# Performance work log

Measured on AMD Instinct MI355X. Metric: run time of the kernel, lower is better.

The kernel has to match this reference:

```python
import jax, jax.numpy as jnp
import numpy as np
from jax import lax

# Dimensions (must match input_specs)
B, T, C = 2, 2048, 1024
H = 4 * C          # FFN hidden
E_RWKV, E_TRANS = 6, 2
E = E_RWKV + E_TRANS
LN_EPS = 1e-5


def layernorm(x, g, b):
    m = x.mean(-1, keepdims=True)
    v = ((x - m) ** 2).mean(-1, keepdims=True)
    return (x - m) * lax.rsqrt(v + LN_EPS) * g + b


def setup_inputs() -> dict:
    key = jax.random.key(0)
    ks = jax.random.split(key, 24)
    s = 0.02
    inp = {
        "x": jax.random.normal(ks[0], (B, T, C), jnp.float32),
        "v_first": jax.random.normal(ks[1], (B, T, C), jnp.float32),
        "winners": jax.random.randint(ks[2], (B, T, 2), 0, E),
        "capital_shares": jax.random.uniform(ks[3], (E,), jnp.float32),
        # LayerNorms
        "ln1_g": jnp.ones((C,), jnp.float32), "ln1_b": jnp.zeros((C,), jnp.float32),
        "ln2_g": jnp.ones((C,), jnp.float32), "ln2_b": jnp.zeros((C,), jnp.float32),
        # RWKV-style time-mix (simplified RWKV7_TimeMix)
        "Wr": s * jax.random.normal(ks[4], (C, C), jnp.float32),
        "Wk": s * jax.random.normal(ks[5], (C, C), jnp.float32),
        "Wv": s * jax.random.normal(ks[6], (C, C), jnp.float32),
        "Wo": s * jax.random.normal(ks[7], (C, C), jnp.float32),
        "w_decay": jax.random.normal(ks[8], (C,), jnp.float32),
        "g_v": jax.random.normal(ks[9], (C,), jnp.float32),
        # bridge: linear on concat(h, rwkv_state)
        "Wb": s * jax.random.normal(ks[10], (2 * C, C), jnp.float32),
        "bb": jnp.zeros((C,), jnp.float32),
        # 6 stacked SparseRWKVFFN experts: sigmoid(x Wr_r) * (relu(x Wk_r)^2 Wv_r)
        "Wk_r": s * jax.random.normal(ks[11], (E_RWKV, C, H), jnp.float32),
        "Wv_r": s * jax.random.normal(ks[12], (E_RWKV, H, C), jnp.float32),
        "Wr_r": s * jax.random.normal(ks[13], (E_RWKV, C, C), jnp.float32),
        # 2 stacked LinearTransformerExpert: gelu((h+prefix) W1) W2
        "W1_t": s * jax.random.normal(ks[14], (E_TRANS, C, H), jnp.float32),
        "W2_t": s * jax.random.normal(ks[15], (E_TRANS, H, C), jnp.float32),
    }
    return inp


def reference(x, v_first, winners, capital_shares,
              ln1_g, ln1_b, ln2_g, ln2_b,
              Wr, Wk, Wv, Wo, w_decay, g_v,
              Wb, bb, Wk_r, Wv_r, Wr_r, W1_t, W2_t):
    # ---- attention (simplified RWKV time-mix), returns per-token state ----
    h1 = layernorm(x, ln1_g, ln1_b)
    r = jax.nn.sigmoid(h1 @ Wr)                      # [B,T,C]
    k = h1 @ Wk
    v = h1 @ Wv
    v = v + (v_first - v) * jax.nn.sigmoid(g_v)      # value-residual mix
    w = jax.nn.sigmoid(w_decay)                      # per-channel decay [C]

    def step(s, kv):
        k_t, v_t = kv                                # [B,C] each
        s = w * s + k_t * v_t
        return s, s

    s0 = jnp.zeros((B, C), x.dtype)
    _, states = lax.scan(step, s0, (jnp.swapaxes(k, 0, 1), jnp.swapaxes(v, 0, 1)))
    states = jnp.swapaxes(states, 0, 1)              # rwkv_state [B,T,C]

    att_out = (r * states) @ Wo
    x = x + att_out
    h = layernorm(x, ln2_g, ln2_b)

    # ---- bridge prefix (flat over tokens, vectorized) ----
    bridge_prefix = jnp.concatenate([h, states], axis=-1) @ Wb + bb  # [B,T,C]

    # ---- experts computed densely, combined by top-2 gates ----
    # RWKV FFN experts
    a = jnp.square(jax.nn.relu(jnp.einsum('btc,ech->ebth', h, Wk_r)))     # [Er,B,T,H]
    rec = jax.nn.sigmoid(jnp.einsum('btc,ecd->ebtd', h, Wr_r))            # [Er,B,T,C]
    out_r = rec * jnp.einsum('ebth,ehc->ebtc', a, Wv_r)                   # [Er,B,T,C]
    # Linear-transformer experts consume the bridge prefix
    ht = h + bridge_prefix
    out_t = jnp.einsum('ebth,ehc->ebtc',
                       jax.nn.gelu(jnp.einsum('btc,ech->ebth', ht, W1_t)),
                       W2_t)                                              # [Et,B,T,C]
    all_out = jnp.concatenate([out_r, out_t], axis=0)                     # [E,B,T,C]

    # top-2 combine, each rank weighted 0.5 (use_market=False branch)
    gate = 0.5 * (jax.nn.one_hot(winners[..., 0], E, dtype=x.dtype)
                  + jax.nn.one_hot(winners[..., 1], E, dtype=x.dtype))    # [B,T,E]
    final_out = jnp.einsum('ebtc,bte->btc', all_out, gate)

    return x + final_out
```

## Files before the change

### kernel.cpp

```cpp
#include <hip/hip_runtime.h>

typedef unsigned short u16;
typedef __bf16 bf16x8 __attribute__((ext_vector_type(8)));
typedef float f32x4 __attribute__((ext_vector_type(4)));

__device__ __forceinline__ float bf2f(u16 u){ union{unsigned i;float f;}x; x.i=((unsigned)u)<<16; return x.f; }
__device__ __forceinline__ u16 f2bf(float f){ union{float f;unsigned i;}x; x.f=f; unsigned r = x.i + 0x7FFFu + ((x.i>>16)&1u); return (u16)(r>>16); }
__device__ __forceinline__ float sigm(float x){ return 1.f/(1.f+expf(-x)); }

struct __align__(8) U16x4 { u16 v[4]; };

#define PSTRIDE 8388608ull

struct CJob { const float* src; u16* dst; int K, N, base; };
struct CJobs { CJob j[27]; };

__global__ void conv_all(CJobs cj){
  __shared__ u16 tile[128][65];
  int id = blockIdx.x;
  int sel = 0;
  #pragma unroll
  for (int i=1;i<27;++i) if (cj.j[i].base <= id) sel = i;
  const float* __restrict__ src = cj.j[sel].src;
  u16* __restrict__ dst = cj.j[sel].dst;
  int K = cj.j[sel].K, N = cj.j[sel].N;
  int lt = id - cj.j[sel].base;
  int tn = N >> 6;
  int k0 = (lt / tn) * 128, n0 = (lt % tn) * 64;
  int tid = threadIdx.x;
  #pragma unroll
  for (int it=0; it<8; ++it){
    int e = it*1024 + tid*4;
    int r = e>>6, c = e&63;
    float4 v = *(const float4*)(src + (size_t)(k0+r)*N + n0 + c);
    tile[r][c+0]=f2bf(v.x); tile[r][c+1]=f2bf(v.y); tile[r][c+2]=f2bf(v.z); tile[r][c+3]=f2bf(v.w);
  }
  __syncthreads();
  #pragma unroll
  for (int it=0; it<8; ++it){
    int e = it*1024 + tid*4;
    int n = e>>7, k = e&127;
    U16x4 o;
    #pragma unroll
    for (int j=0;j<4;++j) o.v[j] = tile[k+j][n];
    *(U16x4*)(dst + (size_t)(n0+n)*K + k0 + k) = o;
  }
}

__global__ void ln_k(const float* __restrict__ x, const float* __restrict__ g, const float* __restrict__ b,
                     u16* __restrict__ out, int ostride){
  int row = blockIdx.x, tid = threadIdx.x;
  float4 v = *(const float4*)(x + (size_t)row*1024 + tid*4);
  float s = v.x+v.y+v.z+v.w;
  float ss = v.x*v.x+v.y*v.y+v.z*v.z+v.w*v.w;
  #pragma unroll
  for (int o=32;o;o>>=1){ s += __shfl_down(s,o); ss += __shfl_down(ss,o); }
  __shared__ float sm[8];
  int lane = tid&63, wv = tid>>6;
  if (!lane){ sm[wv]=s; sm[4+wv]=ss; }
  __syncthreads();
  s = sm[0]+sm[1]+sm[2]+sm[3]; ss = sm[4]+sm[5]+sm[6]+sm[7];
  float mean = s*(1.f/1024.f);
  float var = ss*(1.f/1024.f) - mean*mean;
  float inv = rsqrtf(var + 1e-5f);
  U16x4 o;
  const float* vp = &v.x;
  #pragma unroll
  for (int j=0;j<4;++j){
    int c = tid*4+j;
    o.v[j] = f2bf((vp[j]-mean)*inv*g[c] + b[c]);
  }
  *(U16x4*)(out + (size_t)row*ostride + tid*4) = o;
}

__global__ void red_x_ln(const float* __restrict__ x, const u16* __restrict__ part,
                         const float* __restrict__ g, const float* __restrict__ b,
                         float* __restrict__ out, u16* __restrict__ hcat){
  int row = blockIdx.x, tid = threadIdx.x;
  size_t i = (size_t)row*1024 + tid*4;
  U16x4 p0 = *(const U16x4*)(part + i);
  U16x4 p1 = *(const U16x4*)(part + PSTRIDE + i);
  float4 xv = *(const float4*)(x + i);
  float4 v;
  v.x = xv.x + bf2f(p0.v[0]) + bf2f(p1.v[0]);
  v.y = xv.y + bf2f(p0.v[1]) + bf2f(p1.v[1]);
  v.z = xv.z + bf2f(p0.v[2]) + bf2f(p1.v[2]);
  v.w = xv.w + bf2f(p0.v[3]) + bf2f(p1.v[3]);
  *(float4*)(out + i) = v;
  float s = v.x+v.y+v.z+v.w;
  float ss = v.x*v.x+v.y*v.y+v.z*v.z+v.w*v.w;
  #pragma unroll
  for (int o=32;o;o>>=1){ s += __shfl_down(s,o); ss += __shfl_down(ss,o); }
  __shared__ float sm[8];
  int lane = tid&63, wv = tid>>6;
  if (!lane){ sm[wv]=s; sm[4+wv]=ss; }
  __syncthreads();
  s = sm[0]+sm[1]+sm[2]+sm[3]; ss = sm[4]+sm[5]+sm[6]+sm[7];
  float mean = s*(1.f/1024.f);
  float var = ss*(1.f/1024.f) - mean*mean;
  float inv = rsqrtf(var + 1e-5f);
  U16x4 o;
  const float* vp = &v.x;
  #pragma unroll
  for (int j=0;j<4;++j){
    int c = tid*4+j;
    o.v[j] = f2bf((vp[j]-mean)*inv*g[c] + b[c]);
  }
  *(U16x4*)(hcat + (size_t)row*2048 + tid*4) = o;
}

__global__ void scan_p1(const u16* __restrict__ kbuf, const u16* __restrict__ vbuf,
                        const float* __restrict__ w_decay, float* __restrict__ carry){
  int c = blockIdx.x*256 + threadIdx.x;
  int chunk = blockIdx.y, b = blockIdx.z;
  float w = sigm(w_decay[c]);
  float s = 0.f;
  size_t idx = ((size_t)(b*2048 + chunk*64))*1024 + c;
  #pragma unroll 4
  for (int i=0;i<64;++i){ s = w*s + bf2f(kbuf[idx])*bf2f(vbuf[idx]); idx += 1024; }
  carry[((size_t)(b*32+chunk))*1024 + c] = s;
}
__global__ void scan_p2(const float* __restrict__ w_decay, const float* __restrict__ carry,
                        float* __restrict__ startv){
  int c = blockIdx.x*256 + threadIdx.x;
  int b = blockIdx.y;
  float w = sigm(w_decay[c]);
  float wL = w;
  #pragma unroll
  for (int i=0;i<6;++i) wL *= wL;
  float p = 0.f;
  for (int j=0;j<32;++j){
    size_t id = ((size_t)(b*32+j))*1024 + c;
    startv[id] = p;
    p = wL*p + carry[id];
  }
}
__global__ void scan_p3(const u16* __restrict__ kbuf, const u16* __restrict__ vbuf, const u16* __restrict__ rbuf,
                        const float* __restrict__ w_decay, const float* __restrict__ startv,
                        u16* __restrict__ rs, u16* __restrict__ hcat){
  int c = blockIdx.x*256 + threadIdx.x;
  int chunk = blockIdx.y, b = blockIdx.z;
  float w = sigm(w_decay[c]);
  float s = startv[((size_t)(b*32+chunk))*1024 + c];
  size_t t0 = (size_t)b*2048 + chunk*64;
  size_t idx = t0*1024 + c;
  size_t idx2 = t0*2048 + 1024 + c;
  for (int i=0;i<64;++i){
    s = w*s + bf2f(kbuf[idx])*bf2f(vbuf[idx]);
    rs[idx] = f2bf(bf2f(rbuf[idx]) * s);
    hcat[idx2] = f2bf(s);
    idx += 1024; idx2 += 2048;
  }
}

__global__ void route_count(const int* __restrict__ winners, int* __restrict__ offs, int* __restrict__ cursor){
  __shared__ int cnt[8];
  if (threadIdx.x < 8) cnt[threadIdx.x] = 0;
  __syncthreads();
  for (int p = threadIdx.x; p < 8192; p += 256) atomicAdd(&cnt[winners[p]&7], 1);
  __syncthreads();
  if (threadIdx.x == 0){
    int s = 0;
    #pragma unroll
    for (int e=0;e<8;++e){ offs[e]=s; s+=cnt[e]; }
    offs[8]=s;
  }
  if (threadIdx.x < 8) cursor[threadIdx.x] = 0;
}
__global__ void route_scatter(const int* __restrict__ winners, const int* __restrict__ offs,
                              int* __restrict__ cursor, int* __restrict__ idx_all){
  int p = blockIdx.x*256 + threadIdx.x;
  if (p < 8192){
    int e = winners[p]&7;
    int pos = offs[e] + atomicAdd(&cursor[e], 1);
    idx_all[pos] = p>>1;
  }
}

struct GArgs {
  const u16* A; const u16* B;
  long long lda, bstride;
  int K, Mdense, eBase, nxt, kdiv;
  const int* offs; const int* idx_all;
  const float* v_first; const float* g_v;
  u16* rbuf; u16* kbuf; u16* vbuf;
  u16* act; u16* part;
};

#define GLL(gp, lp) __builtin_amdgcn_global_load_lds((const __attribute__((address_space(1))) void*)(gp), \
                                                     (__attribute__((address_space(3))) void*)(lp), 16, 0, 0)

template<int EPI, int GATHER>
__global__ __launch_bounds__(256,3) void gemm_k(GArgs g){
  int e = g.eBase + blockIdx.z;
  int rbase = 0, m = g.Mdense;
  if (g.offs){ rbase = g.offs[e]; m = g.offs[e+1] - rbase; }
  if ((int)blockIdx.y * 128 >= m) return;
  const int xt = (int)blockIdx.x % g.nxt;
  const int ksplit = (int)blockIdx.x / g.nxt;
  const long long kOff = (long long)ksplit * g.kdiv;
  __shared__ char smem[49152];
  const int tid = threadIdx.x, lane = tid&63, wave = tid>>6;
  const int wr = wave>>1, wc = wave&1;
  const int nk = g.kdiv >> 5;

  const int srowi = tid>>2;
  const long long scol = (long long)((tid&3)*8);

  const u16* bBase0 = g.B + (long long)blockIdx.z*g.bstride
                    + ((long long)(xt*128) + srowi)*(long long)g.K + kOff + scol;
  const u16* bBase1 = bBase0 + 64ll*(long long)g.K;

  int aRd[4], bRd[4];
  #pragma unroll
  for (int q=0;q<4;++q){
    aRd[q] = (wr*64 + q*16 + (lane&15))*64 + (lane>>4)*16;
    bRd[q] = 8192 + (wc*64 + q*16 + (lane&15))*64 + (lane>>4)*16;
  }

  for (int mt = blockIdx.y; mt*128 < m; mt += gridDim.y){
    const u16 *aP0, *aP1;
    {
      int g0 = mt*128 + srowi;       g0 = g0 < m ? g0 : m-1;
      int g1 = mt*128 + 64 + srowi;  g1 = g1 < m ? g1 : m-1;
      long long r0, r1;
      if (GATHER){ r0 = g.idx_all[rbase+g0]; r1 = g.idx_all[rbase+g1]; }
      else if (g.offs){ r0 = rbase+g0; r1 = rbase+g1; }
      else { r0 = g0; r1 = g1; }
      aP0 = g.A + r0*g.lda + kOff + scol;
      aP1 = g.A + r1*g.lda + kOff + scol;
    }
    const u16* bP0 = bBase0;
    const u16* bP1 = bBase1;

    f32x4 acc[4][4];
    #pragma unroll
    for (int mm=0;mm<4;++mm)
      #pragma unroll
      for (int nn=0;nn<4;++nn)
        acc[mm][nn] = f32x4{0.f,0.f,0.f,0.f};

    #define STAGE(BUF) do{ \
      char* db = smem + (BUF)*16384 + wave*1024; \
      GLL(aP0, db); GLL(aP1, db+4096); GLL(bP0, db+8192); GLL(bP1, db+12288); \
      aP0+=32; aP1+=32; bP0+=32; bP1+=32; }while(0)

    STAGE(0); STAGE(1);
    int bufC = 0, bufS = 2;
    for (int ks=0; ks<nk; ++ks){
      if (ks+2 < nk){
        STAGE(bufS); bufS = bufS==2 ? 0 : bufS+1;
        asm volatile("s_waitcnt vmcnt(8)" ::: "memory");
      } else if (ks+1 < nk){
        asm volatile("s_waitcnt vmcnt(4)" ::: "memory");
      } else {
        asm volatile("s_waitcnt vmcnt(0)" ::: "memory");
      }
      asm volatile("s_barrier" ::: "memory");
      const char* base = smem + bufC*16384;
      bf16x8 af[4], bfv[4];
      #pragma unroll
      for (int q=0;q<4;++q) af[q] = *(const bf16x8*)(base + aRd[q]);
      #pragma unroll
      for (int q=0;q<4;++q) bfv[q] = *(const bf16x8*)(base + bRd[q]);
      #pragma unroll
      for (int mm=0;mm<4;++mm)
        #pragma unroll
        for (int nn=0;nn<4;++nn)
          acc[mm][nn] = __builtin_amdgcn_mfma_f32_16x16x32_bf16(af[mm], bfv[nn], acc[mm][nn], 0,0,0);
      asm volatile("s_waitcnt lgkmcnt(0)" ::: "memory");
      asm volatile("s_barrier" ::: "memory");
      bufC = bufC==2 ? 0 : bufC+1;
    }
    #undef STAGE

    int colB = xt*128 + wc*64 + (lane&15);
    #pragma unroll
    for (int mm=0;mm<4;++mm){
      #pragma unroll
      for (int j=0;j<4;++j){
        int grow = mt*128 + wr*64 + mm*16 + (lane>>4)*4 + j;
        if (grow >= m) continue;
        size_t gr = (size_t)(rbase + grow);
        #pragma unroll
        for (int nn=0;nn<4;++nn){
          int col = colB + nn*16;
          float val = acc[mm][nn][j];
          if (EPI==0){
            if (col < 1024) g.rbuf[gr*1024+col] = f2bf(sigm(val));
            else if (col < 2048) g.kbuf[gr*1024+col-1024] = f2bf(val);
            else {
              int c2 = col-2048;
              float sg = sigm(g.g_v[c2]);
              float vf = g.v_first[gr*1024+c2];
              g.vbuf[gr*1024+c2] = f2bf(val + (vf-val)*sg);
            }
          } else if (EPI==3){
            float r_ = fmaxf(val, 0.f);
            g.act[gr*4096+col] = f2bf(r_*r_);
          } else if (EPI==6){
            float t3 = val*val*val;
            float th = tanhf(0.79788456080286535588f*(val + 0.044715f*t3));
            g.act[gr*4096+col] = f2bf(0.5f*val*(1.f+th));
          } else {
            g.part[(size_t)ksplit*PSTRIDE + gr*1024 + col] = f2bf(val);
          }
        }
      }
    }
  }
}

__global__ void red_ht(const u16* __restrict__ hcat, const u16* __restrict__ part,
                       const float* __restrict__ bb, u16* __restrict__ ht){
  int c = threadIdx.x*4;
  size_t i = (size_t)blockIdx.x*1024 + c;
  U16x4 p0 = *(const U16x4*)(part + i);
  U16x4 p1 = *(const U16x4*)(part + PSTRIDE + i);
  U16x4 hv = *(const U16x4*)(hcat + (size_t)blockIdx.x*2048 + c);
  U16x4 o;
  #pragma unroll
  for (int j=0;j<4;++j) o.v[j] = f2bf(bf2f(hv.v[j]) + bf2f(p0.v[j]) + bf2f(p1.v[j]) + bb[c+j]);
  *(U16x4*)(ht + i) = o;
}
__global__ void red_moe(const int* __restrict__ offs, const int* __restrict__ idx_all,
                        const u16* __restrict__ part, float* __restrict__ out){
  int gr = blockIdx.x;
  if (gr >= offs[8]) return;
  int tok = idx_all[gr];
  bool isr = gr < offs[6];
  int c = threadIdx.x*4;
  size_t i = (size_t)gr*1024 + c;
  U16x4 p0 = *(const U16x4*)(part + i);
  U16x4 p1 = *(const U16x4*)(part + PSTRIDE + i);
  U16x4 r0, r1;
  if (isr){ r0 = *(const U16x4*)(part + 2*PSTRIDE + i); r1 = *(const U16x4*)(part + 3*PSTRIDE + i); }
  #pragma unroll
  for (int j=0;j<4;++j){
    float s = bf2f(p0.v[j]) + bf2f(p1.v[j]);
    float v;
    if (isr){ float rc = sigm(bf2f(r0.v[j]) + bf2f(r1.v[j])); v = 0.5f*s*rc; }
    else v = 0.5f*s;
    atomicAdd(&out[(size_t)tok*1024 + c + j], v);
  }
}

extern "C" void kernel_launch(void* const* d_in, const int* in_sizes, int n_in,
                              void* d_out, int out_size, void* d_ws, size_t ws_size,
                              hipStream_t stream) {
  const float* x       = (const float*)d_in[0];
  const float* v_first = (const float*)d_in[1];
  const int*   winners = (const int*)d_in[2];
  const float* ln1_g   = (const float*)d_in[4];
  const float* ln1_b   = (const float*)d_in[5];
  const float* ln2_g   = (const float*)d_in[6];
  const float* ln2_b   = (const float*)d_in[7];
  const float* Wr      = (const float*)d_in[8];
  const float* Wk      = (const float*)d_in[9];
  const float* Wv      = (const float*)d_in[10];
  const float* Wo      = (const float*)d_in[11];
  const float* w_decay = (const float*)d_in[12];
  const float* g_v     = (const float*)d_in[13];
  const float* Wb      = (const float*)d_in[14];
  const float* bb      = (const float*)d_in[15];
  const float* Wk_r    = (const float*)d_in[16];
  const float* Wv_r    = (const float*)d_in[17];
  const float* Wr_r    = (const float*)d_in[18];
  const float* W1_t    = (const float*)d_in[19];
  const float* W2_t    = (const float*)d_in[20];
  float* out = (float*)d_out;

  char* p = (char*)d_ws;
  auto alloc = [&](size_t bytes)->char*{ char* r=p; p += (bytes+255)&~(size_t)255; return r; };
  u16* wTrkv = (u16*)alloc(3072ull*1024*2);
  u16* wTo   = (u16*)alloc(1024ull*1024*2);
  u16* wTb   = (u16*)alloc(1024ull*2048*2);
  u16* wTkr  = (u16*)alloc(6ull*4096*1024*2);
  u16* wTvr  = (u16*)alloc(6ull*1024*4096*2);
  u16* wTrr  = (u16*)alloc(6ull*1024*1024*2);
  u16* wT1   = (u16*)alloc(2ull*4096*1024*2);
  u16* wT2   = (u16*)alloc(2ull*1024*4096*2);
  u16* h1    = (u16*)alloc(4096ull*1024*2);
  u16* rbuf  = (u16*)alloc(4096ull*1024*2);
  u16* kbuf  = (u16*)alloc(4096ull*1024*2);
  u16* vbuf  = (u16*)alloc(4096ull*1024*2);
  u16* rsb   = (u16*)alloc(4096ull*1024*2);
  u16* hcat  = (u16*)alloc(4096ull*2048*2);
  u16* htb   = (u16*)alloc(4096ull*1024*2);
  u16* act   = (u16*)alloc(8192ull*4096*2);
  u16* partial = (u16*)alloc(4ull*8192*1024*2);
  float* carry  = (float*)alloc(2ull*32*1024*4);
  float* startv = (float*)alloc(2ull*32*1024*4);
  int* offs   = (int*)alloc(16*4);
  int* cursor = (int*)alloc(8*4);
  int* idx_all= (int*)alloc(8192*4);

  dim3 B256(256);

  {
    CJobs cj; int base = 0, ji = 0;
    auto add = [&](const float* s, u16* d, int K, int N){
      cj.j[ji++] = CJob{s, d, K, N, base}; base += (K>>7)*(N>>6);
    };
    add(Wr, wTrkv, 1024,1024); add(Wk, wTrkv+1024*1024, 1024,1024);
    add(Wv, wTrkv+2048*1024, 1024,1024); add(Wo, wTo, 1024,1024);
    add(Wb, wTb, 2048,1024);
    for (int e2=0;e2<6;++e2) add(Wk_r + (size_t)e2*1024*4096, wTkr + (size_t)e2*4096*1024, 1024,4096);
    for (int e2=0;e2<6;++e2) add(Wv_r + (size_t)e2*4096*1024, wTvr + (size_t)e2*1024*4096, 4096,1024);
    for (int e2=0;e2<6;++e2) add(Wr_r + (size_t)e2*1024*1024, wTrr + (size_t)e2*1024*1024, 1024,1024);
    for (int e2=0;e2<2;++e2) add(W1_t + (size_t)e2*1024*4096, wT1 + (size_t)e2*4096*1024, 1024,4096);
    for (int e2=0;e2<2;++e2) add(W2_t + (size_t)e2*4096*1024, wT2 + (size_t)e2*1024*4096, 4096,1024);
    conv_all<<<dim3(base,1,1),B256,0,stream>>>(cj);
  }

  route_count<<<1,B256,0,stream>>>(winners, offs, cursor);
  route_scatter<<<32,B256,0,stream>>>(winners, offs, cursor, idx_all);

  ln_k<<<4096,B256,0,stream>>>(x, ln1_g, ln1_b, h1, 1024);

  {
    GArgs ga{}; ga.A=h1; ga.B=wTrkv; ga.lda=1024; ga.K=1024; ga.Mdense=4096; ga.nxt=24; ga.kdiv=1024;
    ga.v_first=v_first; ga.g_v=g_v; ga.rbuf=rbuf; ga.kbuf=kbuf; ga.vbuf=vbuf;
    gemm_k<0,0><<<dim3(24,32,1),B256,0,stream>>>(ga);
  }

  scan_p1<<<dim3(4,32,2),B256,0,stream>>>(kbuf, vbuf, w_decay, carry);
  scan_p2<<<dim3(4,2,1), B256,0,stream>>>(w_decay, carry, startv);
  scan_p3<<<dim3(4,32,2),B256,0,stream>>>(kbuf, vbuf, rbuf, w_decay, startv, rsb, hcat);

  {
    GArgs ga{}; ga.A=rsb; ga.B=wTo; ga.lda=1024; ga.K=1024; ga.Mdense=4096; ga.nxt=8; ga.kdiv=512;
    ga.part=partial;
    gemm_k<1,0><<<dim3(16,32,1),B256,0,stream>>>(ga);
  }
  red_x_ln<<<4096,B256,0,stream>>>(x, partial, ln2_g, ln2_b, out, hcat);

  {
    GArgs ga{}; ga.A=hcat; ga.B=wTb; ga.lda=2048; ga.K=2048; ga.Mdense=4096; ga.nxt=8; ga.kdiv=1024;
    ga.part=partial;
    gemm_k<2,0><<<dim3(16,32,1),B256,0,stream>>>(ga);
  }
  red_ht<<<4096,B256,0,stream>>>(hcat, partial, bb, htb);

  {
    GArgs ga{}; ga.A=hcat; ga.B=wTkr; ga.lda=2048; ga.bstride=4096ll*1024; ga.K=1024; ga.nxt=32; ga.kdiv=1024;
    ga.offs=offs; ga.eBase=0; ga.idx_all=idx_all; ga.act=act;
    gemm_k<3,1><<<dim3(32,12,6),B256,0,stream>>>(ga);
  }
  {
    GArgs ga{}; ga.A=hcat; ga.B=wTrr; ga.lda=2048; ga.bstride=1024ll*1024; ga.K=1024; ga.nxt=8; ga.kdiv=512;
    ga.offs=offs; ga.eBase=0; ga.idx_all=idx_all; ga.part=partial + 2*PSTRIDE;
    gemm_k<4,1><<<dim3(16,12,6),B256,0,stream>>>(ga);
  }
  {
    GArgs ga{}; ga.A=act; ga.B=wTvr; ga.lda=4096; ga.bstride=1024ll*4096; ga.K=4096; ga.nxt=8; ga.kdiv=2048;
    ga.offs=offs; ga.eBase=0; ga.part=partial;
    gemm_k<5,0><<<dim3(16,12,6),B256,0,stream>>>(ga);
  }
  {
    GArgs ga{}; ga.A=htb; ga.B=wT1; ga.lda=1024; ga.bstride=4096ll*1024; ga.K=1024; ga.nxt=32; ga.kdiv=1024;
    ga.offs=offs; ga.eBase=6; ga.idx_all=idx_all; ga.act=act;
    gemm_k<6,1><<<dim3(32,16,2),B256,0,stream>>>(ga);
  }
  {
    GArgs ga{}; ga.A=act; ga.B=wT2; ga.lda=4096; ga.bstride=1024ll*4096; ga.K=4096; ga.nxt=8; ga.kdiv=2048;
    ga.offs=offs; ga.eBase=6; ga.part=partial;
    gemm_k<7,0><<<dim3(16,16,2),B256,0,stream>>>(ga);
  }
  red_moe<<<8192,B256,0,stream>>>(offs, idx_all, partial, out);

  (void)in_sizes; (void)n_in; (void)out_size; (void)ws_size;
}
```

Baseline: 729.6 us.

## Use 256-row GEMM tiles with 512-thread blocks and 4-way split-K for transformer down-proj

The GEMM kernel moves from 256-thread blocks with 128x128 tiles to 512-thread blocks with 256x128 tiles. Eight waves now share one B tile staged in LDS, so each B load is reused across twice as many rows, and LDS grows to 72KB. Grid y dimensions are halved to match. The transformer expert down-projection switches to 4-way split-K writing all four partial buffers, and red_moe now sums four partials for non-RWKV rows. The larger LDS footprint and 512-thread blocks lower occupancy, and the larger tile raises padding waste for small expert row counts.

```diff
diff --git a/kernel.cpp b/kernel.cpp
--- a/kernel.cpp
+++ b/kernel.cpp
@@ -191,15 +191,15 @@
                                                      (__attribute__((address_space(3))) void*)(lp), 16, 0, 0)
 
 template<int EPI, int GATHER>
-__global__ __launch_bounds__(256,3) void gemm_k(GArgs g){
+__global__ __launch_bounds__(512,4) void gemm_k(GArgs g){
   int e = g.eBase + blockIdx.z;
   int rbase = 0, m = g.Mdense;
   if (g.offs){ rbase = g.offs[e]; m = g.offs[e+1] - rbase; }
-  if ((int)blockIdx.y * 128 >= m) return;
+  if ((int)blockIdx.y * 256 >= m) return;
   const int xt = (int)blockIdx.x % g.nxt;
   const int ksplit = (int)blockIdx.x / g.nxt;
   const long long kOff = (long long)ksplit * g.kdiv;
-  __shared__ char smem[49152];
+  __shared__ char smem[73728];
   const int tid = threadIdx.x, lane = tid&63, wave = tid>>6;
   const int wr = wave>>1, wc = wave&1;
   const int nk = g.kdiv >> 5;
@@ -209,20 +209,19 @@
 
   const u16* bBase0 = g.B + (long long)blockIdx.z*g.bstride
                     + ((long long)(xt*128) + srowi)*(long long)g.K + kOff + scol;
-  const u16* bBase1 = bBase0 + 64ll*(long long)g.K;
 
   int aRd[4], bRd[4];
   #pragma unroll
   for (int q=0;q<4;++q){
     aRd[q] = (wr*64 + q*16 + (lane&15))*64 + (lane>>4)*16;
-    bRd[q] = 8192 + (wc*64 + q*16 + (lane&15))*64 + (lane>>4)*16;
-  }
-
-  for (int mt = blockIdx.y; mt*128 < m; mt += gridDim.y){
+    bRd[q] = 16384 + (wc*64 + q*16 + (lane&15))*64 + (lane>>4)*16;
+  }
+
+  for (int mt = blockIdx.y; mt*256 < m; mt += gridDim.y){
     const u16 *aP0, *aP1;
     {
-      int g0 = mt*128 + srowi;       g0 = g0 < m ? g0 : m-1;
-      int g1 = mt*128 + 64 + srowi;  g1 = g1 < m ? g1 : m-1;
+      int g0 = mt*256 + srowi;       g0 = g0 < m ? g0 : m-1;
+      int g1 = mt*256 + 128 + srowi; g1 = g1 < m ? g1 : m-1;
       long long r0, r1;
       if (GATHER){ r0 = g.idx_all[rbase+g0]; r1 = g.idx_all[rbase+g1]; }
       else if (g.offs){ r0 = rbase+g0; r1 = rbase+g1; }
@@ -231,7 +230,6 @@
       aP1 = g.A + r1*g.lda + kOff + scol;
     }
     const u16* bP0 = bBase0;
-    const u16* bP1 = bBase1;
 
     f32x4 acc[4][4];
     #pragma unroll
@@ -241,23 +239,23 @@
         acc[mm][nn] = f32x4{0.f,0.f,0.f,0.f};
 
     #define STAGE(BUF) do{ \
-      char* db = smem + (BUF)*16384 + wave*1024; \
-      GLL(aP0, db); GLL(aP1, db+4096); GLL(bP0, db+8192); GLL(bP1, db+12288); \
-      aP0+=32; aP1+=32; bP0+=32; bP1+=32; }while(0)
+      char* db = smem + (BUF)*24576 + wave*1024; \
+      GLL(aP0, db); GLL(aP1, db+8192); GLL(bP0, db+16384); \
+      aP0+=32; aP1+=32; bP0+=32; }while(0)
 
     STAGE(0); STAGE(1);
     int bufC = 0, bufS = 2;
     for (int ks=0; ks<nk; ++ks){
       if (ks+2 < nk){
         STAGE(bufS); bufS = bufS==2 ? 0 : bufS+1;
-        asm volatile("s_waitcnt vmcnt(8)" ::: "memory");
+        asm volatile("s_waitcnt vmcnt(6)" ::: "memory");
       } else if (ks+1 < nk){
-        asm volatile("s_waitcnt vmcnt(4)" ::: "memory");
+        asm volatile("s_waitcnt vmcnt(3)" ::: "memory");
       } else {
         asm volatile("s_waitcnt vmcnt(0)" ::: "memory");
       }
       asm volatile("s_barrier" ::: "memory");
-      const char* base = smem + bufC*16384;
+      const char* base = smem + bufC*24576;
       bf16x8 af[4], bfv[4];
       #pragma unroll
       for (int q=0;q<4;++q) af[q] = *(const bf16x8*)(base + aRd[q]);
@@ -279,7 +277,7 @@
     for (int mm=0;mm<4;++mm){
       #pragma unroll
       for (int j=0;j<4;++j){
-        int grow = mt*128 + wr*64 + mm*16 + (lane>>4)*4 + j;
+        int grow = mt*256 + wr*64 + mm*16 + (lane>>4)*4 + j;
         if (grow >= m) continue;
         size_t gr = (size_t)(rbase + grow);
         #pragma unroll
@@ -333,14 +331,17 @@
   size_t i = (size_t)gr*1024 + c;
   U16x4 p0 = *(const U16x4*)(part + i);
   U16x4 p1 = *(const U16x4*)(part + PSTRIDE + i);
-  U16x4 r0, r1;
-  if (isr){ r0 = *(const U16x4*)(part + 2*PSTRIDE + i); r1 = *(const U16x4*)(part + 3*PSTRIDE + i); }
+  U16x4 p2 = *(const U16x4*)(part + 2*PSTRIDE + i);
+  U16x4 p3 = *(const U16x4*)(part + 3*PSTRIDE + i);
   #pragma unroll
   for (int j=0;j<4;++j){
-    float s = bf2f(p0.v[j]) + bf2f(p1.v[j]);
     float v;
-    if (isr){ float rc = sigm(bf2f(r0.v[j]) + bf2f(r1.v[j])); v = 0.5f*s*rc; }
-    else v = 0.5f*s;
+    if (isr){
+      float rc = sigm(bf2f(p2.v[j]) + bf2f(p3.v[j]));
+      v = 0.5f*(bf2f(p0.v[j]) + bf2f(p1.v[j]))*rc;
+    } else {
+      v = 0.5f*(bf2f(p0.v[j]) + bf2f(p1.v[j]) + bf2f(p2.v[j]) + bf2f(p3.v[j]));
+    }
     atomicAdd(&out[(size_t)tok*1024 + c + j], v);
   }
 }
@@ -395,7 +396,7 @@
   int* cursor = (int*)alloc(8*4);
   int* idx_all= (int*)alloc(8192*4);
 
-  dim3 B256(256);
+  dim3 B256(256), B512(512);
 
   {
     CJobs cj; int base = 0, ji = 0;
@@ -421,7 +422,7 @@
   {
     GArgs ga{}; ga.A=h1; ga.B=wTrkv; ga.lda=1024; ga.K=1024; ga.Mdense=4096; ga.nxt=24; ga.kdiv=1024;
     ga.v_first=v_first; ga.g_v=g_v; ga.rbuf=rbuf; ga.kbuf=kbuf; ga.vbuf=vbuf;
-    gemm_k<0,0><<<dim3(24,32,1),B256,0,stream>>>(ga);
+    gemm_k<0,0><<<dim3(24,16,1),B512,0,stream>>>(ga);
   }
 
   scan_p1<<<dim3(4,32,2),B256,0,stream>>>(kbuf, vbuf, w_decay, carry);
@@ -431,41 +432,41 @@
   {
     GArgs ga{}; ga.A=rsb; ga.B=wTo; ga.lda=1024; ga.K=1024; ga.Mdense=4096; ga.nxt=8; ga.kdiv=512;
     ga.part=partial;
-    gemm_k<1,0><<<dim3(16,32,1),B256,0,stream>>>(ga);
+    gemm_k<1,0><<<dim3(16,16,1),B512,0,stream>>>(ga);
   }
   red_x_ln<<<4096,B256,0,stream>>>(x, partial, ln2_g, ln2_b, out, hcat);
 
   {
     GArgs ga{}; ga.A=hcat; ga.B=wTb; ga.lda=2048; ga.K=2048; ga.Mdense=4096; ga.nxt=8; ga.kdiv=1024;
     ga.part=partial;
-    gemm_k<2,0><<<dim3(16,32,1),B256,0,stream>>>(ga);
+    gemm_k<2,0><<<dim3(16,16,1),B512,0,stream>>>(ga);
   }
   red_ht<<<4096,B256,0,stream>>>(hcat, partial, bb, htb);
 
   {
     GArgs ga{}; ga.A=hcat; ga.B=wTkr; ga.lda=2048; ga.bstride=4096ll*1024; ga.K=1024; ga.nxt=32; ga.kdiv=1024;
     ga.offs=offs; ga.eBase=0; ga.idx_all=idx_all; ga.act=act;
-    gemm_k<3,1><<<dim3(32,12,6),B256,0,stream>>>(ga);
+    gemm_k<3,1><<<dim3(32,6,6),B512,0,stream>>>(ga);
   }
   {
     GArgs ga{}; ga.A=hcat; ga.B=wTrr; ga.lda=2048; ga.bstride=1024ll*1024; ga.K=1024; ga.nxt=8; ga.kdiv=512;
     ga.offs=offs; ga.eBase=0; ga.idx_all=idx_all; ga.part=partial + 2*PSTRIDE;
-    gemm_k<4,1><<<dim3(16,12,6),B256,0,stream>>>(ga);
+    gemm_k<4,1><<<dim3(16,6,6),B512,0,stream>>>(ga);
   }
   {
     GArgs ga{}; ga.A=act; ga.B=wTvr; ga.lda=4096; ga.bstride=1024ll*4096; ga.K=4096; ga.nxt=8; ga.kdiv=2048;
     ga.offs=offs; ga.eBase=0; ga.part=partial;
-    gemm_k<5,0><<<dim3(16,12,6),B256,0,stream>>>(ga);
+    gemm_k<5,0><<<dim3(16,6,6),B512,0,stream>>>(ga);
   }
   {
     GArgs ga{}; ga.A=htb; ga.B=wT1; ga.lda=1024; ga.bstride=4096ll*1024; ga.K=1024; ga.nxt=32; ga.kdiv=1024;
     ga.offs=offs; ga.eBase=6; ga.idx_all=idx_all; ga.act=act;
-    gemm_k<6,1><<<dim3(32,16,2),B256,0,stream>>>(ga);
-  }
-  {
-    GArgs ga{}; ga.A=act; ga.B=wT2; ga.lda=4096; ga.bstride=1024ll*4096; ga.K=4096; ga.nxt=8; ga.kdiv=2048;
+    gemm_k<6,1><<<dim3(32,4,2),B512,0,stream>>>(ga);
+  }
+  {
+    GArgs ga{}; ga.A=act; ga.B=wT2; ga.lda=4096; ga.bstride=1024ll*4096; ga.K=4096; ga.nxt=8; ga.kdiv=1024;
     ga.offs=offs; ga.eBase=6; ga.part=partial;
-    gemm_k<7,0><<<dim3(16,16,2),B256,0,stream>>>(ga);
+    gemm_k<7,0><<<dim3(32,4,2),B512,0,stream>>>(ga);
   }
   red_moe<<<8192,B256,0,stream>>>(offs, idx_all, partial, out);
 
```

Result: slower. 749.1 us (+2.7%).

## Merge five per-expert MoE GEMM launches into two grouped launches

Applied to the files above, without the earlier changes.

Replaces five separate expert GEMM launches (RWKV key, receptance, value, and transformer W1/W2) with two grouped kernels. The first handles all up-projections plus receptance and the second all down-projections, with the expert and epilogue chosen from blockIdx.z. The transformer down-projection now uses a 4-way K split, and red_moe sums four partials for those rows. The goal is to cut launch count and tail idle time by running independent expert GEMMs concurrently, at the cost of runtime epilogue branching and a fixed y-grid of 6 that loops over M tiles.

```diff
diff --git a/kernel.cpp b/kernel.cpp
--- a/kernel.cpp
+++ b/kernel.cpp
@@ -295,13 +295,134 @@
               float vf = g.v_first[gr*1024+c2];
               g.vbuf[gr*1024+c2] = f2bf(val + (vf-val)*sg);
             }
-          } else if (EPI==3){
+          } else {
+            g.part[(size_t)ksplit*PSTRIDE + gr*1024 + col] = f2bf(val);
+          }
+        }
+      }
+    }
+  }
+}
+
+struct MoeArgs {
+  const u16* hcat; const u16* htb; const u16* act;
+  const u16* wTkr; const u16* wT1; const u16* wTrr; const u16* wTvr; const u16* wT2;
+  const int* offs; const int* idx_all;
+  u16* actw; u16* part;
+};
+
+template<int PHASE>
+__global__ __launch_bounds__(256,3) void gemm_moe(MoeArgs g){
+  int z = blockIdx.z;
+  const u16 *Ap, *Bp; long long lda; int K, kdiv, nxt, e, epi;
+  if (PHASE==0){
+    if (z < 6){ e=z;   Ap=g.hcat; lda=2048; Bp=g.wTkr + (long long)z*4096*1024;     K=1024; kdiv=1024; nxt=32; epi=0; }
+    else if (z < 8){ e=z; Ap=g.htb; lda=1024; Bp=g.wT1 + (long long)(z-6)*4096*1024; K=1024; kdiv=1024; nxt=32; epi=1; }
+    else { e=z-8; Ap=g.hcat; lda=2048; Bp=g.wTrr + (long long)(z-8)*1024*1024;      K=1024; kdiv=512;  nxt=8;  epi=2; }
+  } else {
+    if (z < 6){ e=z; Ap=g.act; lda=4096; Bp=g.wTvr + (long long)z*1024*4096;        K=4096; kdiv=2048; nxt=8;  epi=3; }
+    else { e=z;     Ap=g.act; lda=4096; Bp=g.wT2 + (long long)(z-6)*1024*4096;      K=4096; kdiv=1024; nxt=8;  epi=4; }
+  }
+  if ((int)blockIdx.x >= nxt * (K / kdiv)) return;
+  int rbase = g.offs[e], m = g.offs[e+1] - rbase;
+  if ((int)blockIdx.y * 128 >= m) return;
+  const int xt = (int)blockIdx.x % nxt;
+  const int ksplit = (int)blockIdx.x / nxt;
+  const long long kOff = (long long)ksplit * kdiv;
+  __shared__ char smem[49152];
+  const int tid = threadIdx.x, lane = tid&63, wave = tid>>6;
+  const int wr = wave>>1, wc = wave&1;
+  const int nk = kdiv >> 5;
+
+  const int srowi = tid>>2;
+  const long long scol = (long long)((tid&3)*8);
+
+  const u16* bBase0 = Bp + ((long long)(xt*128) + srowi)*(long long)K + kOff + scol;
+  const u16* bBase1 = bBase0 + 64ll*(long long)K;
+
+  int aRd[4], bRd[4];
+  #pragma unroll
+  for (int q=0;q<4;++q){
+    aRd[q] = (wr*64 + q*16 + (lane&15))*64 + (lane>>4)*16;
+    bRd[q] = 8192 + (wc*64 + q*16 + (lane&15))*64 + (lane>>4)*16;
+  }
+
+  for (int mt = blockIdx.y; mt*128 < m; mt += gridDim.y){
+    const u16 *aP0, *aP1;
+    {
+      int g0 = mt*128 + srowi;       g0 = g0 < m ? g0 : m-1;
+      int g1 = mt*128 + 64 + srowi;  g1 = g1 < m ? g1 : m-1;
+      long long r0, r1;
+      if (epi <= 2){ r0 = g.idx_all[rbase+g0]; r1 = g.idx_all[rbase+g1]; }
+      else { r0 = rbase+g0; r1 = rbase+g1; }
+      aP0 = Ap + r0*lda + kOff + scol;
+      aP1 = Ap + r1*lda + kOff + scol;
+    }
+    const u16* bP0 = bBase0;
+    const u16* bP1 = bBase1;
+
+    f32x4 acc[4][4];
+    #pragma unroll
+    for (int mm=0;mm<4;++mm)
+      #pragma unroll
+      for (int nn=0;nn<4;++nn)
+        acc[mm][nn] = f32x4{0.f,0.f,0.f,0.f};
+
+    #define STAGE(BUF) do{ \
+      char* db = smem + (BUF)*16384 + wave*1024; \
+      GLL(aP0, db); GLL(aP1, db+4096); GLL(bP0, db+8192); GLL(bP1, db+12288); \
+      aP0+=32; aP1+=32; bP0+=32; bP1+=32; }while(0)
+
+    STAGE(0); STAGE(1);
+    int bufC = 0, bufS = 2;
+    for (int ks=0; ks<nk; ++ks){
+      if (ks+2 < nk){
+        STAGE(bufS); bufS = bufS==2 ? 0 : bufS+1;
+        asm volatile("s_waitcnt vmcnt(8)" ::: "memory");
+      } else if (ks+1 < nk){
+        asm volatile("s_waitcnt vmcnt(4)" ::: "memory");
+      } else {
+        asm volatile("s_waitcnt vmcnt(0)" ::: "memory");
+      }
+      asm volatile("s_barrier" ::: "memory");
+      const char* base = smem + bufC*16384;
+      bf16x8 af[4], bfv[4];
+      #pragma unroll
+      for (int q=0;q<4;++q) af[q] = *(const bf16x8*)(base + aRd[q]);
+      #pragma unroll
+      for (int q=0;q<4;++q) bfv[q] = *(const bf16x8*)(base + bRd[q]);
+      #pragma unroll
+      for (int mm=0;mm<4;++mm)
+        #pragma unroll
+        for (int nn=0;nn<4;++nn)
+          acc[mm][nn] = __builtin_amdgcn_mfma_f32_16x16x32_bf16(af[mm], bfv[nn], acc[mm][nn], 0,0,0);
+      asm volatile("s_waitcnt lgkmcnt(0)" ::: "memory");
+      asm volatile("s_barrier" ::: "memory");
+      bufC = bufC==2 ? 0 : bufC+1;
+    }
+    #undef STAGE
+
+    int colB = xt*128 + wc*64 + (lane&15);
+    #pragma unroll
+    for (int mm=0;mm<4;++mm){
+      #pragma unroll
+      for (int j=0;j<4;++j){
+        int grow = mt*128 + wr*64 + mm*16 + (lane>>4)*4 + j;
+        if (grow >= m) continue;
+        size_t gr = (size_t)(rbase + grow);
+        #pragma unroll
+        for (int nn=0;nn<4;++nn){
+          int col = colB + nn*16;
+          float val = acc[mm][nn][j];
+          if (epi == 0){
             float r_ = fmaxf(val, 0.f);
-            g.act[gr*4096+col] = f2bf(r_*r_);
-          } else if (EPI==6){
+            g.actw[gr*4096+col] = f2bf(r_*r_);
+          } else if (epi == 1){
             float t3 = val*val*val;
             float th = tanhf(0.79788456080286535588f*(val + 0.044715f*t3));
-            g.act[gr*4096+col] = f2bf(0.5f*val*(1.f+th));
+            g.actw[gr*4096+col] = f2bf(0.5f*val*(1.f+th));
+          } else if (epi == 2){
+            g.part[(size_t)(2+ksplit)*PSTRIDE + gr*1024 + col] = f2bf(val);
           } else {
             g.part[(size_t)ksplit*PSTRIDE + gr*1024 + col] = f2bf(val);
           }
@@ -333,14 +454,17 @@
   size_t i = (size_t)gr*1024 + c;
   U16x4 p0 = *(const U16x4*)(part + i);
   U16x4 p1 = *(const U16x4*)(part + PSTRIDE + i);
-  U16x4 r0, r1;
-  if (isr){ r0 = *(const U16x4*)(part + 2*PSTRIDE + i); r1 = *(const U16x4*)(part + 3*PSTRIDE + i); }
+  U16x4 p2 = *(const U16x4*)(part + 2*PSTRIDE + i);
+  U16x4 p3 = *(const U16x4*)(part + 3*PSTRIDE + i);
   #pragma unroll
   for (int j=0;j<4;++j){
-    float s = bf2f(p0.v[j]) + bf2f(p1.v[j]);
     float v;
-    if (isr){ float rc = sigm(bf2f(r0.v[j]) + bf2f(r1.v[j])); v = 0.5f*s*rc; }
-    else v = 0.5f*s;
+    if (isr){
+      float rc = sigm(bf2f(p2.v[j]) + bf2f(p3.v[j]));
+      v = 0.5f*(bf2f(p0.v[j]) + bf2f(p1.v[j]))*rc;
+    } else {
+      v = 0.5f*(bf2f(p0.v[j]) + bf2f(p1.v[j]) + bf2f(p2.v[j]) + bf2f(p3.v[j]));
+    }
     atomicAdd(&out[(size_t)tok*1024 + c + j], v);
   }
 }
@@ -443,29 +567,12 @@
   red_ht<<<4096,B256,0,stream>>>(hcat, partial, bb, htb);
 
   {
-    GArgs ga{}; ga.A=hcat; ga.B=wTkr; ga.lda=2048; ga.bstride=4096ll*1024; ga.K=1024; ga.nxt=32; ga.kdiv=1024;
-    ga.offs=offs; ga.eBase=0; ga.idx_all=idx_all; ga.act=act;
-    gemm_k<3,1><<<dim3(32,12,6),B256,0,stream>>>(ga);
-  }
-  {
-    GArgs ga{}; ga.A=hcat; ga.B=wTrr; ga.lda=2048; ga.bstride=1024ll*1024; ga.K=1024; ga.nxt=8; ga.kdiv=512;
-    ga.offs=offs; ga.eBase=0; ga.idx_all=idx_all; ga.part=partial + 2*PSTRIDE;
-    gemm_k<4,1><<<dim3(16,12,6),B256,0,stream>>>(ga);
-  }
-  {
-    GArgs ga{}; ga.A=act; ga.B=wTvr; ga.lda=4096; ga.bstride=1024ll*4096; ga.K=4096; ga.nxt=8; ga.kdiv=2048;
-    ga.offs=offs; ga.eBase=0; ga.part=partial;
-    gemm_k<5,0><<<dim3(16,12,6),B256,0,stream>>>(ga);
-  }
-  {
-    GArgs ga{}; ga.A=htb; ga.B=wT1; ga.lda=1024; ga.bstride=4096ll*1024; ga.K=1024; ga.nxt=32; ga.kdiv=1024;
-    ga.offs=offs; ga.eBase=6; ga.idx_all=idx_all; ga.act=act;
-    gemm_k<6,1><<<dim3(32,16,2),B256,0,stream>>>(ga);
-  }
-  {
-    GArgs ga{}; ga.A=act; ga.B=wT2; ga.lda=4096; ga.bstride=1024ll*4096; ga.K=4096; ga.nxt=8; ga.kdiv=2048;
-    ga.offs=offs; ga.eBase=6; ga.part=partial;
-    gemm_k<7,0><<<dim3(16,16,2),B256,0,stream>>>(ga);
+    MoeArgs ma{};
+    ma.hcat=hcat; ma.htb=htb; ma.act=act;
+    ma.wTkr=wTkr; ma.wT1=wT1; ma.wTrr=wTrr; ma.wTvr=wTvr; ma.wT2=wT2;
+    ma.offs=offs; ma.idx_all=idx_all; ma.actw=act; ma.part=partial;
+    gemm_moe<0><<<dim3(32,6,14),B256,0,stream>>>(ma);
+    gemm_moe<1><<<dim3(32,6,8),B256,0,stream>>>(ma);
   }
   red_moe<<<8192,B256,0,stream>>>(offs, idx_all, partial, out);
 
```

New measurement: 747.5 us. 1.02x slower.
